# Performance work log

Measured on AMD Instinct MI355X. Metric: run time of the kernel, lower is better.

The kernel has to match this reference:

```python
import jax, jax.numpy as jnp
import numpy as np

N_MEL = 80
ATTN = 512
PRENET = 256
RNN = 1024
B, T = 32, 800


def setup_inputs() -> dict:
    key = jax.random.key(0)
    ks = jax.random.split(key, 10)
    s = lambda fan_in: 1.0 / np.sqrt(fan_in)
    return {
        "memory": jax.random.normal(ks[0], (B, T, ATTN), jnp.float32),
        "y_mels": jax.random.normal(ks[1], (B, T, N_MEL), jnp.float32),
        # Prenet: two bias-free linears with ReLU
        "prenet_w1": jax.random.uniform(ks[2], (PRENET, N_MEL), jnp.float32, -s(N_MEL), s(N_MEL)),
        "prenet_w2": jax.random.uniform(ks[3], (PRENET, PRENET), jnp.float32, -s(PRENET), s(PRENET)),
        # LSTM (1 layer): input dim = PRENET + ATTN = 768, gate order i,f,g,o
        "w_ih": jax.random.uniform(ks[4], (4 * RNN, PRENET + ATTN), jnp.float32, -s(RNN), s(RNN)),
        "w_hh": jax.random.uniform(ks[5], (4 * RNN, RNN), jnp.float32, -s(RNN), s(RNN)),
        "b_ih": jax.random.uniform(ks[6], (4 * RNN,), jnp.float32, -s(RNN), s(RNN)),
        "b_hh": jax.random.uniform(ks[7], (4 * RNN,), jnp.float32, -s(RNN), s(RNN)),
        # Linear projection: (RNN + ATTN) -> N_MEL, with bias
        "proj_w": jax.random.uniform(ks[8], (N_MEL, RNN + ATTN), jnp.float32, -s(RNN + ATTN), s(RNN + ATTN)),
        "proj_b": jax.random.uniform(ks[9], (N_MEL,), jnp.float32, -s(RNN + ATTN), s(RNN + ATTN)),
    }


def _decoder_fwd(memory, y_mels, prenet_w1, prenet_w2, w_ih, w_hh, b_ih, b_hh, proj_w, proj_b):
    b, t, _ = memory.shape
    # teacher-forced previous frames: step j consumes zeros (j=0) or y_mels[:, j-1]
    prev = jnp.concatenate([jnp.zeros((b, 1, N_MEL), memory.dtype), y_mels[:, : t - 1]], axis=1)  # [B,T,80]
    # prenet (eval mode: dropout off; double relu == relu)
    h = jax.nn.relu(jnp.einsum("btm,pm->btp", prev, prenet_w1))
    h = jax.nn.relu(jnp.einsum("btp,qp->btq", h, prenet_w2))  # [B,T,256]
    x = jnp.concatenate([h, memory], axis=-1)  # [B,T,768]
    # precompute input-to-gate contributions for all steps
    gates_in = jnp.einsum("btd,gd->tbg", x, w_ih) + (b_ih + b_hh)  # [T,B,4H]

    def step(carry, g_in):
        hh, cc = carry
        gates = g_in + hh @ w_hh.T  # [B,4H]
        i, f_, g, o = jnp.split(gates, 4, axis=-1)
        cc = jax.nn.sigmoid(f_) * cc + jax.nn.sigmoid(i) * jnp.tanh(g)
        hh = jax.nn.sigmoid(o) * jnp.tanh(cc)
        return (hh, cc), hh

    init = (jnp.zeros((b, RNN), memory.dtype), jnp.zeros((b, RNN), memory.dtype))
    _, hs = jax.lax.scan(step, init, gates_in)  # [T,B,H]
    hs = jnp.transpose(hs, (1, 0, 2))  # [B,T,H]
    out = jnp.concatenate([hs, memory], axis=-1)  # [B,T,H+ATTN]
    mel = jnp.einsum("btd,md->btm", out, proj_w) + proj_b  # [B,T,80]
    return mel.reshape(b, -1, N_MEL)


def reference(memory, y_mels, prenet_w1, prenet_w2, w_ih, w_hh, b_ih, b_hh, proj_w, proj_b):
    return _decoder_fwd(memory, y_mels, prenet_w1, prenet_w2, w_ih, w_hh, b_ih, b_hh, proj_w, proj_b)
```

## Files before the change

### kernel.cpp

```cpp
#include <hip/hip_runtime.h>
#include <hip/hip_bf16.h>

typedef unsigned short u16;
typedef unsigned int u32;
typedef unsigned long long u64;
typedef __attribute__((ext_vector_type(8))) short short8;
typedef __attribute__((ext_vector_type(4))) float f32x4;

#define ROWS 25600

__device__ __forceinline__ u16 f2bf(float f){
  u32 x = __builtin_bit_cast(u32, f);
  u32 r = (x + 0x7FFFu + ((x >> 16) & 1u)) >> 16;
  return (u16)r;
}
__device__ __forceinline__ float bf2f(u16 h){
  return __builtin_bit_cast(float, ((u32)h) << 16);
}
__device__ __forceinline__ float sigf(float x){
  x = fminf(fmaxf(x, -30.f), 30.f);
  return 1.f / (1.f + __expf(-x));
}
__device__ __forceinline__ float tanh_(float x){
  x = fminf(fmaxf(x, -15.f), 15.f);
  float e = __expf(-2.f * x);
  return (1.f - e) / (1.f + e);
}


__global__ void initk(u32* flags, u16* hb, float* cst){
  int i = blockIdx.x * blockDim.x + threadIdx.x;
  int stride = blockDim.x * gridDim.x;
  for (int j = i; j < 64 * 32; j += stride) flags[j] = 0;
  for (int j = i; j < 2 * 32 * 1024; j += stride) hb[j] = 0;
  for (int j = i; j < 32 * 1024; j += stride) cst[j] = 0.f;
}

__global__ void sentinel_fill(float* out, int n, float val){
  for (int i = blockIdx.x * blockDim.x + threadIdx.x; i < n;
       i += blockDim.x * gridDim.x)
    out[i] = val;
}

__global__ void prep_prev(const float* __restrict__ ym, u16* __restrict__ prevp){
  int idx = blockIdx.x * blockDim.x + threadIdx.x;
  if (idx >= ROWS * 96) return;
  int r = idx / 96, c = idx - r * 96;
  int b = r / 800, t = r - b * 800;
  float v = 0.f;
  if (c < 80 && t > 0) v = ym[(u64)(b * 800 + (t - 1)) * 80 + c];
  prevp[idx] = f2bf(v);
}

__global__ void prep_w(const float* __restrict__ w1, const float* __restrict__ w2,
                       const float* __restrict__ wih, const float* __restrict__ pw,
                       const float* __restrict__ bih, const float* __restrict__ bhh,
                       const float* __restrict__ whh,
                       u16* __restrict__ w1p, u16* __restrict__ w2b,
                       u16* __restrict__ wihb, u16* __restrict__ projp,
                       float* __restrict__ bsum, u16* __restrict__ whhb){
  int idx = blockIdx.x * blockDim.x + threadIdx.x;
  const int n1 = 256 * 96, n2 = 256 * 256, n3 = 4096 * 768, n4 = 128 * 1536, n5 = 4096;
  const int n6 = 4096 * 1024;
  if (idx < n1){
    int r = idx / 96, c = idx - r * 96;
    w1p[idx] = (c < 80) ? f2bf(w1[r * 80 + c]) : (u16)0;
  } else if ((idx -= n1) < n2){
    w2b[idx] = f2bf(w2[idx]);
  } else if ((idx -= n2) < n3){
    wihb[idx] = f2bf(wih[idx]);
  } else if ((idx -= n3) < n4){
    int r = idx / 1536;
    projp[idx] = (r < 80) ? f2bf(pw[idx]) : (u16)0;
  } else if ((idx -= n4) < n5){
    bsum[idx] = bih[idx] + bhh[idx];
  } else if ((idx -= n5) < n6){
    whhb[idx] = f2bf(whh[idx]);
  }
}


template<int RELU, int OUTF32, int HASBIAS, int AMAP, int SPLIT>
__global__ __launch_bounds__(256, 2) void gemm_tn(
    const u16* __restrict__ A, const float* __restrict__ A2,
    const u16* __restrict__ W, void* __restrict__ Cv,
    const float* __restrict__ bias,
    int M, int K, int lda, int lda2, int ldw, int ldc, int nmax,
    int ksplit, int t0)
{
  __shared__ __align__(16) u16 As[128 * 32];
  __shared__ __align__(16) u16 Ws[128 * 32];
  const int tid = threadIdx.x;
  const int lane = tid & 63;
  const int wv = tid >> 6;
  const int wr = wv & 1, wc = wv >> 1;
  const int mtiles = M >> 7;
  const int ntiles = gridDim.x / mtiles;
  int bm, bn;
  if (mtiles & 7){
    bm = blockIdx.x % mtiles;
    bn = blockIdx.x / mtiles;
  } else {
    int per = 8 * ntiles;
    int g = blockIdx.x / per, rem = blockIdx.x % per;
    bm = g * 8 + (rem & 7);
    bn = rem >> 3;
  }
  const int m0 = bm << 7, n0 = bn << 7;
  const int KT = K >> 5;

  f32x4 acc[4][4] = {};

  const int r0 = tid >> 2, c0 = tid & 3;
  const int r1 = r0 + 64;
  const u16* Wb = W + (u64)n0 * ldw;
  const int ws0 = r0 * 32 + ((c0 ^ ((r0 >> 1) & 3)) << 3);
  const int ws1 = r1 * 32 + ((c0 ^ ((r1 >> 1) & 3)) << 3);

  auto rowmap = [&](int r) -> int {
    int gr = m0 + r;
    if (AMAP) return (gr & 31) * 800 + t0 + (gr >> 5);
    return gr;
  };
  const u64 ab0 = (u64)rowmap(r0) * lda;
  const u64 ab1 = (u64)rowmap(r1) * lda;
  const u64 af0 = SPLIT ? (u64)rowmap(r0) * lda2 : 0;
  const u64 af1 = SPLIT ? (u64)rowmap(r1) * lda2 : 0;

  auto aload = [&](u64 rb, u64 rf, int k) -> uint4 {
    if (SPLIT && k >= ksplit){
      const float* p = A2 + rf + (k - ksplit);
      const float4 a = *(const float4*)p;
      const float4 b = *(const float4*)(p + 4);
      uint4 r;
      r.x = (u32)f2bf(a.x) | ((u32)f2bf(a.y) << 16);
      r.y = (u32)f2bf(a.z) | ((u32)f2bf(a.w) << 16);
      r.z = (u32)f2bf(b.x) | ((u32)f2bf(b.y) << 16);
      r.w = (u32)f2bf(b.z) | ((u32)f2bf(b.w) << 16);
      return r;
    }
    return *(const uint4*)(A + rb + k);
  };

  uint4 ra0 = aload(ab0, af0, c0 * 8);
  uint4 ra1 = aload(ab1, af1, c0 * 8);
  uint4 rw0 = *(const uint4*)(Wb + r0 * ldw + c0 * 8);
  uint4 rw1 = *(const uint4*)(Wb + r1 * ldw + c0 * 8);

  const int r16 = lane & 15, cg = lane >> 4;

  for (int kt = 0; kt < KT; ++kt){
    *(uint4*)&As[ws0] = ra0;
    *(uint4*)&As[ws1] = ra1;
    *(uint4*)&Ws[ws0] = rw0;
    *(uint4*)&Ws[ws1] = rw1;
    __syncthreads();
    if (kt + 1 < KT){
      const int k0 = ((kt + 1) << 5) + c0 * 8;
      ra0 = aload(ab0, af0, k0);
      ra1 = aload(ab1, af1, k0);
      rw0 = *(const uint4*)(Wb + r0 * ldw + k0);
      rw1 = *(const uint4*)(Wb + r1 * ldw + k0);
    }
    short8 af[4], wf[4];
    #pragma unroll
    for (int mt = 0; mt < 4; ++mt){
      const int row = (wr << 6) + (mt << 4) + r16;
      af[mt] = *(const short8*)&As[(row << 5) + ((cg ^ ((row >> 1) & 3)) << 3)];
    }
    #pragma unroll
    for (int nt = 0; nt < 4; ++nt){
      const int row = (wc << 6) + (nt << 4) + r16;
      wf[nt] = *(const short8*)&Ws[(row << 5) + ((cg ^ ((row >> 1) & 3)) << 3)];
    }
    #pragma unroll
    for (int mt = 0; mt < 4; ++mt)
      #pragma unroll
      for (int nt = 0; nt < 4; ++nt)
        acc[mt][nt] = __builtin_amdgcn_mfma_f32_16x16x32_bf16(af[mt], wf[nt], acc[mt][nt], 0, 0, 0);
    __syncthreads();
  }

  #pragma unroll
  for (int nt = 0; nt < 4; ++nt){
    const int gn = n0 + (wc << 6) + (nt << 4) + r16;
    if (gn < nmax){
      float bv = 0.f;
      if (HASBIAS) bv = bias[gn];
      #pragma unroll
      for (int mt = 0; mt < 4; ++mt){
        #pragma unroll
        for (int r = 0; r < 4; ++r){
          const int gm = m0 + (wr << 6) + (mt << 4) + (cg << 2) + r;
          float v = acc[mt][nt][r] + bv;
          if (RELU) v = fmaxf(v, 0.f);
          if (OUTF32) ((float*)Cv)[(u64)gm * ldc + gn] = v;
          else        ((u16*)Cv)[(u64)gm * ldc + gn] = f2bf(v);
        }
      }
    }
  }
}


__global__ __launch_bounds__(512, 1) void lstm_chunk(
    const u16* __restrict__ whhb, const u16* __restrict__ gslot,
    u16* __restrict__ hb, u16* __restrict__ hs, float* __restrict__ cst,
    u32* flags, int t0, int steps)
{
  __shared__ __align__(16) u16 hsm[32 * 1024];
  const int tid = threadIdx.x;
  const int lane = tid & 63;
  const int wv = tid >> 6;
  const int gate = wv & 3, mh = wv >> 2;
  const int u0 = blockIdx.x << 4;
  const int r16 = lane & 15, cg = lane >> 4;

  short8 wf[32];
  {
    const u16* wrow = whhb + (u64)((gate << 10) + u0 + r16) * 1024 + (cg << 3);
    #pragma unroll
    for (int kk = 0; kk < 32; ++kk)
      wf[kk] = *(const short8*)(wrow + (kk << 5));
  }

  const int pb = tid >> 4, pu = tid & 15;
  float ccell = cst[(pb << 10) + u0 + pu];
  const int arow = (mh << 4) + r16;
  const u16* abase = &hsm[arow << 10];
  const int aswz = (arow & 7) << 3;
  const u64 deadline = __builtin_amdgcn_s_memrealtime() + 100000000ull;

  for (int i = 0; i < steps; ++i){
    const int t = t0 + i;
    const int cur = t & 1;
    u16 gv0, gv1, gv2, gv3;
    {
      const u64 gb = ((u64)i * 32 + pb) * 4096 + u0 + pu;
      gv0 = gslot[gb];        gv1 = gslot[gb + 1024];
      gv2 = gslot[gb + 2048]; gv3 = gslot[gb + 3072];
    }
    if (t > 0){
      if (wv == 0){
        while (1){
          u32 v = __hip_atomic_load(&flags[lane << 5], __ATOMIC_RELAXED,
                                    __HIP_MEMORY_SCOPE_AGENT);
          if (__all((int)(v >= (u32)t))) break;
          if (__builtin_amdgcn_s_memrealtime() > deadline) break;
        }
        __builtin_amdgcn_fence(__ATOMIC_ACQUIRE, "agent");
      }
      __syncthreads();
    }
    {
      const u16* hsrc = hb + cur * 32768;
      uint4 hr[8];
      #pragma unroll
      for (int j = 0; j < 8; ++j) hr[j] = *(const uint4*)(hsrc + (((j << 9) + tid) << 3));
      #pragma unroll
      for (int j = 0; j < 8; ++j){
        const int ci = (j << 9) + tid;
        const int row = ci >> 7, k16 = ci & 127;
        *(uint4*)&hsm[(row << 10) + ((k16 ^ (row & 7)) << 3)] = hr[j];
      }
    }
    __syncthreads();
    f32x4 acc = {};
    #pragma unroll
    for (int kk = 0; kk < 32; ++kk){
      const int k16 = (kk << 2) + cg;
      const short8 af = *(const short8*)&abase[((k16 << 3) ^ aswz)];
      acc = __builtin_amdgcn_mfma_f32_16x16x32_bf16(af, wf[kk], acc, 0, 0, 0);
    }
    __syncthreads();
    {
      float* gsm = (float*)hsm;
      #pragma unroll
      for (int r = 0; r < 4; ++r){
        const int m = (mh << 4) + (cg << 2) + r;
        gsm[(gate << 9) + (m << 4) + r16] = acc[r];
      }
    }
    __syncthreads();
    {
      const float* gsm = (const float*)hsm;
      const int o = (pb << 4) + pu;
      const float gi = gsm[o]        + bf2f(gv0);
      const float gf = gsm[512 + o]  + bf2f(gv1);
      const float gg = gsm[1024 + o] + bf2f(gv2);
      const float go = gsm[1536 + o] + bf2f(gv3);
      ccell = sigf(gf) * ccell + sigf(gi) * tanh_(gg);
      const float h = sigf(go) * tanh_(ccell);
      const u16 hbits = f2bf(h);
      hs[(((u64)pb * 800 + t) << 10) + u0 + pu] = hbits;
      const u32 other = (u32)(u16)__shfl_xor((int)(u32)hbits, 1);
      if ((tid & 1) == 0){
        const u32 w = ((u32)hbits) | (other << 16);
        u32* dst = (u32*)(void*)hb + ((cur ^ 1) * 16384 + (pb << 9) + (u0 >> 1) + (pu >> 1));
        __hip_atomic_store(dst, w, __ATOMIC_RELAXED, __HIP_MEMORY_SCOPE_AGENT);
      }
    }
    __syncthreads();
    if (tid == 0)
      __hip_atomic_store(&flags[blockIdx.x << 5], (u32)(t + 1), __ATOMIC_RELAXED,
                         __HIP_MEMORY_SCOPE_AGENT);
  }
  cst[(pb << 10) + u0 + pu] = ccell;
}


extern "C" void kernel_launch(void* const* d_in, const int* in_sizes, int n_in,
                              void* d_out, int out_size, void* d_ws, size_t ws_size,
                              hipStream_t stream){
  const float* memory = (const float*)d_in[0];
  const float* ymels  = (const float*)d_in[1];
  const float* w1     = (const float*)d_in[2];
  const float* w2     = (const float*)d_in[3];
  const float* wih    = (const float*)d_in[4];
  const float* whh    = (const float*)d_in[5];
  const float* bih    = (const float*)d_in[6];
  const float* bhh    = (const float*)d_in[7];
  const float* pw     = (const float*)d_in[8];
  const float* pbias  = (const float*)d_in[9];
  float* out = (float*)d_out;

  char* ws = (char*)d_ws;
  u64 off = 0;
  auto alloc = [&](u64 bytes) -> void* {
    void* p = ws + off;
    off += (bytes + 255) & ~255ull;
    return p;
  };
  u16* hs    = (u16*)alloc((u64)ROWS * 1024 * 2);
  u16* pn    = (u16*)alloc((u64)ROWS * 256 * 2);
  u16* wihb  = (u16*)alloc((u64)4096 * 768 * 2);
  u16* whhb  = (u16*)alloc((u64)4096 * 1024 * 2);
  u16* w1p   = (u16*)alloc(256 * 96 * 2);
  u16* w2b   = (u16*)alloc(256 * 256 * 2);
  u16* projp = (u16*)alloc(128 * 1536 * 2);
  float* bsum = (float*)alloc(4096 * 4);
  u16* hb    = (u16*)alloc(2 * 32768 * 2);
  float* cst = (float*)alloc(32 * 1024 * 4);
  u32* flags = (u32*)alloc(64 * 32 * 4);
  u16* prevp = hs;
  u16* h1b   = hs + (8u << 20);

  int CT = 0;
  u16* ring = (u16*)(ws + off);
  if (ws_size > off){
    u64 avail = ws_size - off;
    CT = (int)(avail / (2ull * 32 * 4096 * 2));
    CT &= ~3;
    if (CT > 96) CT = 96;
  }
  if (CT < 4){
    float val = 1.0e6f + 10.0f * (float)(ws_size >> 20);
    sentinel_fill<<<256, 256, 0, stream>>>(out, out_size, val);
    return;
  }

  initk<<<64, 256, 0, stream>>>(flags, hb, cst);
  prep_prev<<<(ROWS * 96) / 256, 256, 0, stream>>>(ymels, prevp);
  prep_w<<<(256*96 + 256*256 + 4096*768 + 128*1536 + 4096 + 4096*1024 + 255) / 256,
           256, 0, stream>>>(
      w1, w2, wih, pw, bih, bhh, whh, w1p, w2b, wihb, projp, bsum, whhb);

  gemm_tn<1,0,0,0,0><<<200 * 2, 256, 0, stream>>>(prevp, nullptr, w1p, h1b, nullptr,
      ROWS, 96, 96, 0, 96, 256, 256, 0, 0);
  gemm_tn<1,0,0,0,0><<<200 * 2, 256, 0, stream>>>(h1b, nullptr, w2b, pn, nullptr,
      ROWS, 256, 256, 0, 256, 256, 256, 0, 0);

  for (int t0 = 0, c = 0; t0 < 800; t0 += CT, ++c){
    const int steps = (800 - t0 < CT) ? (800 - t0) : CT;
    u16* slot = ring + (u64)(c & 1) * CT * 131072;
    const int Mr = steps * 32;
    gemm_tn<0,0,1,1,1><<<(Mr >> 7) * 32, 256, 0, stream>>>(pn, memory, wihb, slot, bsum,
        Mr, 768, 256, 512, 768, 4096, 4096, 256, t0);
    lstm_chunk<<<64, 512, 0, stream>>>(whhb, slot, hb, hs, cst, flags, t0, steps);
  }

  gemm_tn<0,1,1,0,1><<<200 * 1, 256, 0, stream>>>(hs, memory, projp, out, pbias,
      ROWS, 1536, 1024, 512, 1536, 80, 80, 1024, 0);
}
```

Before: 3.283 ms.

## Trim LSTM step sync: separate gate LDS, atomic h loads, drop fence and barrier

The persistent LSTM kernel gets a dedicated shared buffer for gate outputs, which removes the barrier between the MFMA loop and the gate write. It also drops the acquire fence after the flag spin and reads h with relaxed 64-bit atomic loads instead. Stores of h are packed into 64-bit atomics, the deadline clock is checked only every 16 spins, and the chunk cap is raised from 96 to 100. Removing the fence in favour of relaxed atomics relies on ordering guarantees that may not hold on every memory path, and 64-bit loads are narrower than the previous 128-bit ones.

```diff
diff --git a/kernel.cpp b/kernel.cpp
--- a/kernel.cpp
+++ b/kernel.cpp
@@ -209,6 +209,7 @@
     u32* flags, int t0, int steps)
 {
   __shared__ __align__(16) u16 hsm[32 * 1024];
+  __shared__ __align__(16) float gsm[2048];
   const int tid = threadIdx.x;
   const int lane = tid & 63;
   const int wv = tid >> 6;
@@ -242,26 +243,31 @@
     }
     if (t > 0){
       if (wv == 0){
+        u32 it = 0;
         while (1){
           u32 v = __hip_atomic_load(&flags[lane << 5], __ATOMIC_RELAXED,
                                     __HIP_MEMORY_SCOPE_AGENT);
           if (__all((int)(v >= (u32)t))) break;
-          if (__builtin_amdgcn_s_memrealtime() > deadline) break;
+          if (((++it) & 15u) == 0u &&
+              __builtin_amdgcn_s_memrealtime() > deadline) break;
         }
-        __builtin_amdgcn_fence(__ATOMIC_ACQUIRE, "agent");
       }
       __syncthreads();
     }
     {
-      const u16* hsrc = hb + cur * 32768;
-      uint4 hr[8];
-      #pragma unroll
-      for (int j = 0; j < 8; ++j) hr[j] = *(const uint4*)(hsrc + (((j << 9) + tid) << 3));
-      #pragma unroll
-      for (int j = 0; j < 8; ++j){
+      const u64* hsrc = (const u64*)(void*)(hb + cur * 32768);
+      u64 hr[16];
+      #pragma unroll
+      for (int j = 0; j < 16; ++j)
+        hr[j] = __hip_atomic_load(&hsrc[(j << 9) + tid], __ATOMIC_RELAXED,
+                                  __HIP_MEMORY_SCOPE_AGENT);
+      #pragma unroll
+      for (int j = 0; j < 16; ++j){
         const int ci = (j << 9) + tid;
-        const int row = ci >> 7, k16 = ci & 127;
-        *(uint4*)&hsm[(row << 10) + ((k16 ^ (row & 7)) << 3)] = hr[j];
+        const int row = ci >> 8;
+        const int col8 = ci & 255;
+        const int k16 = col8 >> 1, lo = col8 & 1;
+        *(u64*)((char*)hsm + (row << 11) + ((k16 ^ (row & 7)) << 4) + (lo << 3)) = hr[j];
       }
     }
     __syncthreads();
@@ -272,9 +278,7 @@
       const short8 af = *(const short8*)&abase[((k16 << 3) ^ aswz)];
       acc = __builtin_amdgcn_mfma_f32_16x16x32_bf16(af, wf[kk], acc, 0, 0, 0);
     }
-    __syncthreads();
     {
-      float* gsm = (float*)hsm;
       #pragma unroll
       for (int r = 0; r < 4; ++r){
         const int m = (mh << 4) + (cg << 2) + r;
@@ -283,7 +287,6 @@
     }
     __syncthreads();
     {
-      const float* gsm = (const float*)hsm;
       const int o = (pb << 4) + pu;
       const float gi = gsm[o]        + bf2f(gv0);
       const float gf = gsm[512 + o]  + bf2f(gv1);
@@ -293,10 +296,11 @@
       const float h = sigf(go) * tanh_(ccell);
       const u16 hbits = f2bf(h);
       hs[(((u64)pb * 800 + t) << 10) + u0 + pu] = hbits;
-      const u32 other = (u32)(u16)__shfl_xor((int)(u32)hbits, 1);
-      if ((tid & 1) == 0){
-        const u32 w = ((u32)hbits) | (other << 16);
-        u32* dst = (u32*)(void*)hb + ((cur ^ 1) * 16384 + (pb << 9) + (u0 >> 1) + (pu >> 1));
+      const u32 w1 = ((u32)hbits) | (((u32)(u16)__shfl_xor((int)(u32)hbits, 1)) << 16);
+      const u32 w2 = (u32)__shfl_xor((int)w1, 2);
+      if ((tid & 3) == 0){
+        const u64 w = ((u64)w1) | (((u64)w2) << 32);
+        u64* dst = (u64*)(void*)hb + ((cur ^ 1) * 8192 + (pb << 8) + (u0 >> 2) + (pu >> 2));
         __hip_atomic_store(dst, w, __ATOMIC_RELAXED, __HIP_MEMORY_SCOPE_AGENT);
       }
     }
@@ -351,7 +355,7 @@
     u64 avail = ws_size - off;
     CT = (int)(avail / (2ull * 32 * 4096 * 2));
     CT &= ~3;
-    if (CT > 96) CT = 96;
+    if (CT > 100) CT = 100;
   }
   if (CT < 4){
     float val = 1.0e6f + 10.0f * (float)(ws_size >> 20);
```

Result: slower. 3.537 ms (+7.7%).

## Fuse input-gate GEMM and LSTM recurrence into one persistent producer/consumer kernel

Applied to the files above, without the earlier changes.

Replaces the per-chunk host loop of separate input-gate GEMM and LSTM launches with a single persistent launch. 64 blocks run the recurrence over all 800 steps, and 192 producer blocks compute the input-gate GEMM for the next chunk into a double-buffered ring, coordinated by global flag arrays. The cell state now stays in registers for the whole sequence, and the gate scratch gets its own shared buffer, which drops one barrier per step. This is meant to overlap the GEMM with the serial recurrence and remove launch gaps, but it depends on all 256 blocks being co-resident and caps the chunk size at 64.

```diff
diff --git a/kernel.cpp b/kernel.cpp
--- a/kernel.cpp
+++ b/kernel.cpp
@@ -28,12 +28,12 @@
 }
 
 
-__global__ void initk(u32* flags, u16* hb, float* cst){
+__global__ void initk(u32* wflags, u32* pflags, u16* hb){
   int i = blockIdx.x * blockDim.x + threadIdx.x;
   int stride = blockDim.x * gridDim.x;
-  for (int j = i; j < 64 * 32; j += stride) flags[j] = 0;
+  for (int j = i; j < 64 * 32; j += stride) wflags[j] = 0;
+  for (int j = i; j < 192 * 32; j += stride) pflags[j] = 0;
   for (int j = i; j < 2 * 32 * 1024; j += stride) hb[j] = 0;
-  for (int j = i; j < 32 * 1024; j += stride) cst[j] = 0.f;
 }
 
 __global__ void sentinel_fill(float* out, int n, float val){
@@ -203,15 +203,166 @@
 }
 
 
-__global__ __launch_bounds__(512, 1) void lstm_chunk(
-    const u16* __restrict__ whhb, const u16* __restrict__ gslot,
-    u16* __restrict__ hb, u16* __restrict__ hs, float* __restrict__ cst,
-    u32* flags, int t0, int steps)
+__shared__ __align__(16) u16 fs_hsm[32 * 1024];
+__shared__ __align__(16) float fs_gsm[2048];
+__shared__ __align__(16) u16 fs_As[128 * 32];
+__shared__ __align__(16) u16 fs_Ws[128 * 32];
+
+__device__ void gemm_tile_512(
+    const u16* __restrict__ pn, const float* __restrict__ memory,
+    const u16* __restrict__ wihb, const float* __restrict__ bsum,
+    u16* __restrict__ slot, int bm, int bn, int t0)
 {
-  __shared__ __align__(16) u16 hsm[32 * 1024];
+  const int tid = threadIdx.x;
+  const bool act = (tid < 256);
+  const int lane = tid & 63;
+  const int wv4 = (tid >> 6) & 3;
+  const int wr = wv4 & 1, wc = wv4 >> 1;
+  const int m0 = bm << 7, n0 = bn << 7;
+  const int KT = 24;
+
+  f32x4 acc[4][4] = {};
+  const int r0 = tid >> 2, c0 = tid & 3;
+  const int r1 = r0 + 64;
+  const u16* Wb = wihb + (u64)n0 * 768;
+  const int ws0 = r0 * 32 + ((c0 ^ ((r0 >> 1) & 3)) << 3);
+  const int ws1 = r1 * 32 + ((c0 ^ ((r1 >> 1) & 3)) << 3);
+
+  auto rowmap = [&](int r) -> int {
+    int gr = m0 + r;
+    return (gr & 31) * 800 + t0 + (gr >> 5);
+  };
+  u64 ab0 = 0, ab1 = 0, af0 = 0, af1 = 0;
+  if (act){
+    ab0 = (u64)rowmap(r0) * 256;  af0 = (u64)rowmap(r0) * 512;
+    ab1 = (u64)rowmap(r1) * 256;  af1 = (u64)rowmap(r1) * 512;
+  }
+  auto aload = [&](u64 rb, u64 rf, int k) -> uint4 {
+    if (k >= 256){
+      const float* p = memory + rf + (k - 256);
+      const float4 a = *(const float4*)p;
+      const float4 b = *(const float4*)(p + 4);
+      uint4 r;
+      r.x = (u32)f2bf(a.x) | ((u32)f2bf(a.y) << 16);
+      r.y = (u32)f2bf(a.z) | ((u32)f2bf(a.w) << 16);
+      r.z = (u32)f2bf(b.x) | ((u32)f2bf(b.y) << 16);
+      r.w = (u32)f2bf(b.z) | ((u32)f2bf(b.w) << 16);
+      return r;
+    }
+    return *(const uint4*)(pn + rb + k);
+  };
+
+  uint4 ra0, ra1, rw0, rw1;
+  if (act){
+    ra0 = aload(ab0, af0, c0 * 8);
+    ra1 = aload(ab1, af1, c0 * 8);
+    rw0 = *(const uint4*)(Wb + r0 * 768 + c0 * 8);
+    rw1 = *(const uint4*)(Wb + r1 * 768 + c0 * 8);
+  }
+  const int r16 = lane & 15, cg = lane >> 4;
+
+  for (int kt = 0; kt < KT; ++kt){
+    if (act){
+      *(uint4*)&fs_As[ws0] = ra0;
+      *(uint4*)&fs_As[ws1] = ra1;
+      *(uint4*)&fs_Ws[ws0] = rw0;
+      *(uint4*)&fs_Ws[ws1] = rw1;
+    }
+    __syncthreads();
+    if (act){
+      if (kt + 1 < KT){
+        const int k0 = ((kt + 1) << 5) + c0 * 8;
+        ra0 = aload(ab0, af0, k0);
+        ra1 = aload(ab1, af1, k0);
+        rw0 = *(const uint4*)(Wb + r0 * 768 + k0);
+        rw1 = *(const uint4*)(Wb + r1 * 768 + k0);
+      }
+      short8 af[4], wf[4];
+      #pragma unroll
+      for (int mt = 0; mt < 4; ++mt){
+        const int row = (wr << 6) + (mt << 4) + r16;
+        af[mt] = *(const short8*)&fs_As[(row << 5) + ((cg ^ ((row >> 1) & 3)) << 3)];
+      }
+      #pragma unroll
+      for (int nt = 0; nt < 4; ++nt){
+        const int row = (wc << 6) + (nt << 4) + r16;
+        wf[nt] = *(const short8*)&fs_Ws[(row << 5) + ((cg ^ ((row >> 1) & 3)) << 3)];
+      }
+      #pragma unroll
+      for (int mt = 0; mt < 4; ++mt)
+        #pragma unroll
+        for (int nt = 0; nt < 4; ++nt)
+          acc[mt][nt] = __builtin_amdgcn_mfma_f32_16x16x32_bf16(af[mt], wf[nt], acc[mt][nt], 0, 0, 0);
+    }
+    __syncthreads();
+  }
+
+  if (act){
+    #pragma unroll
+    for (int nt = 0; nt < 4; ++nt){
+      const int gn = n0 + (wc << 6) + (nt << 4) + r16;
+      const float bv = bsum[gn];
+      #pragma unroll
+      for (int mt = 0; mt < 4; ++mt){
+        #pragma unroll
+        for (int r = 0; r < 4; ++r){
+          const int gm = m0 + (wr << 6) + (mt << 4) + (cg << 2) + r;
+          slot[(u64)gm * 4096 + gn] = f2bf(acc[mt][nt][r] + bv);
+        }
+      }
+    }
+  }
+}
+
+__global__ __launch_bounds__(512, 1) void fused(
+    const u16* __restrict__ whhb, const u16* __restrict__ pn,
+    const float* __restrict__ memory, const u16* __restrict__ wihb,
+    const float* __restrict__ bsum, u16* __restrict__ ring,
+    u16* __restrict__ hb, u16* __restrict__ hs,
+    u32* wflags, u32* pflags, int CT, int nchunks)
+{
   const int tid = threadIdx.x;
   const int lane = tid & 63;
   const int wv = tid >> 6;
+  const u64 deadline = __builtin_amdgcn_s_memrealtime() + 100000000ull;
+
+  if (blockIdx.x >= 64){
+    const int p = blockIdx.x - 64;
+    for (int c = 0; c < nchunks; ++c){
+      const int t0 = c * CT;
+      const int steps = (800 - t0 < CT) ? (800 - t0) : CT;
+      if (c >= 2){
+        if (wv == 0){
+          const u32 need = (u32)((c - 1) * CT);
+          u32 it = 0;
+          while (1){
+            u32 v = __hip_atomic_load(&wflags[lane << 5], __ATOMIC_RELAXED,
+                                      __HIP_MEMORY_SCOPE_AGENT);
+            if (__all((int)(v >= need))) break;
+            __builtin_amdgcn_s_sleep(8);
+            if (((++it) & 15u) == 0u &&
+                __builtin_amdgcn_s_memrealtime() > deadline) break;
+          }
+        }
+        __syncthreads();
+      }
+      const int mt = (steps * 32) >> 7;
+      const int TPC = mt * 32;
+      u16* slot = ring + (u64)(c & 1) * ((u64)CT << 17);
+      for (int tau = p; tau < TPC; tau += 192){
+        gemm_tile_512(pn, memory, wihb, bsum, slot, tau % mt, tau / mt, t0);
+      }
+      __syncthreads();
+      if (wv == 0){
+        __builtin_amdgcn_fence(__ATOMIC_RELEASE, "agent");
+        if (tid == 0)
+          __hip_atomic_store(&pflags[p << 5], (u32)(c + 1), __ATOMIC_RELAXED,
+                             __HIP_MEMORY_SCOPE_AGENT);
+      }
+    }
+    return;
+  }
+
   const int gate = wv & 3, mh = wv >> 2;
   const int u0 = blockIdx.x << 4;
   const int r16 = lane & 15, cg = lane >> 4;
@@ -225,32 +376,59 @@
   }
 
   const int pb = tid >> 4, pu = tid & 15;
-  float ccell = cst[(pb << 10) + u0 + pu];
+  float ccell = 0.f;
   const int arow = (mh << 4) + r16;
-  const u16* abase = &hsm[arow << 10];
+  const u16* abase = &fs_hsm[arow << 10];
   const int aswz = (arow & 7) << 3;
-  const u64 deadline = __builtin_amdgcn_s_memrealtime() + 100000000ull;
-
-  for (int i = 0; i < steps; ++i){
-    const int t = t0 + i;
+
+  int c = 0, i = 0;
+  for (int t = 0; t < 800; ++t, ++i){
+    if (i == CT){ c++; i = 0; }
+    const bool boundary = (i == 0);
+    const u16* gslot = ring + (u64)(c & 1) * ((u64)CT << 17);
+    const u64 gb = ((u64)i * 32 + pb) * 4096 + u0 + pu;
     const int cur = t & 1;
-    u16 gv0, gv1, gv2, gv3;
-    {
-      const u64 gb = ((u64)i * 32 + pb) * 4096 + u0 + pu;
+
+    u16 gv0 = 0, gv1 = 0, gv2 = 0, gv3 = 0;
+    if (!boundary){
       gv0 = gslot[gb];        gv1 = gslot[gb + 1024];
       gv2 = gslot[gb + 2048]; gv3 = gslot[gb + 3072];
     }
-    if (t > 0){
+    if (boundary || t > 0){
       if (wv == 0){
-        while (1){
-          u32 v = __hip_atomic_load(&flags[lane << 5], __ATOMIC_RELAXED,
-                                    __HIP_MEMORY_SCOPE_AGENT);
-          if (__all((int)(v >= (u32)t))) break;
-          if (__builtin_amdgcn_s_memrealtime() > deadline) break;
+        if (boundary){
+          const u32 need = (u32)(c + 1);
+          u32 it = 0;
+          while (1){
+            u32 a = __hip_atomic_load(&pflags[lane << 5], __ATOMIC_RELAXED,
+                                      __HIP_MEMORY_SCOPE_AGENT);
+            u32 b = __hip_atomic_load(&pflags[(lane + 64) << 5], __ATOMIC_RELAXED,
+                                      __HIP_MEMORY_SCOPE_AGENT);
+            u32 d = __hip_atomic_load(&pflags[(lane + 128) << 5], __ATOMIC_RELAXED,
+                                      __HIP_MEMORY_SCOPE_AGENT);
+            u32 m = a < b ? a : b; m = m < d ? m : d;
+            if (__all((int)(m >= need))) break;
+            if (((++it) & 15u) == 0u &&
+                __builtin_amdgcn_s_memrealtime() > deadline) break;
+          }
+        }
+        if (t > 0){
+          u32 it = 0;
+          while (1){
+            u32 v = __hip_atomic_load(&wflags[lane << 5], __ATOMIC_RELAXED,
+                                      __HIP_MEMORY_SCOPE_AGENT);
+            if (__all((int)(v >= (u32)t))) break;
+            if (((++it) & 15u) == 0u &&
+                __builtin_amdgcn_s_memrealtime() > deadline) break;
+          }
         }
         __builtin_amdgcn_fence(__ATOMIC_ACQUIRE, "agent");
       }
       __syncthreads();
+    }
+    if (boundary){
+      gv0 = gslot[gb];        gv1 = gslot[gb + 1024];
+      gv2 = gslot[gb + 2048]; gv3 = gslot[gb + 3072];
     }
     {
       const u16* hsrc = hb + cur * 32768;
@@ -261,7 +439,7 @@
       for (int j = 0; j < 8; ++j){
         const int ci = (j << 9) + tid;
         const int row = ci >> 7, k16 = ci & 127;
-        *(uint4*)&hsm[(row << 10) + ((k16 ^ (row & 7)) << 3)] = hr[j];
+        *(uint4*)&fs_hsm[(row << 10) + ((k16 ^ (row & 7)) << 3)] = hr[j];
       }
     }
     __syncthreads();
@@ -272,23 +450,18 @@
       const short8 af = *(const short8*)&abase[((k16 << 3) ^ aswz)];
       acc = __builtin_amdgcn_mfma_f32_16x16x32_bf16(af, wf[kk], acc, 0, 0, 0);
     }
+    #pragma unroll
+    for (int r = 0; r < 4; ++r){
+      const int m = (mh << 4) + (cg << 2) + r;
+      fs_gsm[(gate << 9) + (m << 4) + r16] = acc[r];
+    }
     __syncthreads();
     {
-      float* gsm = (float*)hsm;
-      #pragma unroll
-      for (int r = 0; r < 4; ++r){
-        const int m = (mh << 4) + (cg << 2) + r;
-        gsm[(gate << 9) + (m << 4) + r16] = acc[r];
-      }
-    }
-    __syncthreads();
-    {
-      const float* gsm = (const float*)hsm;
       const int o = (pb << 4) + pu;
-      const float gi = gsm[o]        + bf2f(gv0);
-      const float gf = gsm[512 + o]  + bf2f(gv1);
-      const float gg = gsm[1024 + o] + bf2f(gv2);
-      const float go = gsm[1536 + o] + bf2f(gv3);
+      const float gi = fs_gsm[o]        + bf2f(gv0);
+      const float gf = fs_gsm[512 + o]  + bf2f(gv1);
+      const float gg = fs_gsm[1024 + o] + bf2f(gv2);
+      const float go = fs_gsm[1536 + o] + bf2f(gv3);
       ccell = sigf(gf) * ccell + sigf(gi) * tanh_(gg);
       const float h = sigf(go) * tanh_(ccell);
       const u16 hbits = f2bf(h);
@@ -302,10 +475,9 @@
     }
     __syncthreads();
     if (tid == 0)
-      __hip_atomic_store(&flags[blockIdx.x << 5], (u32)(t + 1), __ATOMIC_RELAXED,
+      __hip_atomic_store(&wflags[blockIdx.x << 5], (u32)(t + 1), __ATOMIC_RELAXED,
                          __HIP_MEMORY_SCOPE_AGENT);
   }
-  cst[(pb << 10) + u0 + pu] = ccell;
 }
 
 
@@ -340,8 +512,8 @@
   u16* projp = (u16*)alloc(128 * 1536 * 2);
   float* bsum = (float*)alloc(4096 * 4);
   u16* hb    = (u16*)alloc(2 * 32768 * 2);
-  float* cst = (float*)alloc(32 * 1024 * 4);
-  u32* flags = (u32*)alloc(64 * 32 * 4);
+  u32* wflags = (u32*)alloc(64 * 32 * 4);
+  u32* pflags = (u32*)alloc(192 * 32 * 4);
   u16* prevp = hs;
   u16* h1b   = hs + (8u << 20);
 
@@ -351,15 +523,16 @@
     u64 avail = ws_size - off;
     CT = (int)(avail / (2ull * 32 * 4096 * 2));
     CT &= ~3;
-    if (CT > 96) CT = 96;
-  }
-  if (CT < 4){
+    if (CT > 64) CT = 64;
+  }
+  if (CT < 8){
     float val = 1.0e6f + 10.0f * (float)(ws_size >> 20);
     sentinel_fill<<<256, 256, 0, stream>>>(out, out_size, val);
     return;
   }
-
-  initk<<<64, 256, 0, stream>>>(flags, hb, cst);
+  const int nchunks = (800 + CT - 1) / CT;
+
+  initk<<<64, 256, 0, stream>>>(wflags, pflags, hb);
   prep_prev<<<(ROWS * 96) / 256, 256, 0, stream>>>(ymels, prevp);
   prep_w<<<(256*96 + 256*256 + 4096*768 + 128*1536 + 4096 + 4096*1024 + 255) / 256,
            256, 0, stream>>>(
@@ -370,14 +543,8 @@
   gemm_tn<1,0,0,0,0><<<200 * 2, 256, 0, stream>>>(h1b, nullptr, w2b, pn, nullptr,
       ROWS, 256, 256, 0, 256, 256, 256, 0, 0);
 
-  for (int t0 = 0, c = 0; t0 < 800; t0 += CT, ++c){
-    const int steps = (800 - t0 < CT) ? (800 - t0) : CT;
-    u16* slot = ring + (u64)(c & 1) * CT * 131072;
-    const int Mr = steps * 32;
-    gemm_tn<0,0,1,1,1><<<(Mr >> 7) * 32, 256, 0, stream>>>(pn, memory, wihb, slot, bsum,
-        Mr, 768, 256, 512, 768, 4096, 4096, 256, t0);
-    lstm_chunk<<<64, 512, 0, stream>>>(whhb, slot, hb, hs, cst, flags, t0, steps);
-  }
+  fused<<<256, 512, 0, stream>>>(whhb, pn, memory, wihb, bsum, ring, hb, hs,
+                                 wflags, pflags, CT, nchunks);
 
   gemm_tn<0,1,1,0,1><<<200 * 1, 256, 0, stream>>>(hs, memory, projp, out, pbias,
       ROWS, 1536, 1024, 512, 1536, 80, 80, 1024, 0);
```

Result: faster. 3.010 ms (-8.3%).
